# Optimization experiments

Hardware: AMD Instinct MI355X
Metric: run time of the kernel (lower is better)

The kernel has to match this reference:

```python
import jax, jax.numpy as jnp
import numpy as np

N_NODES = 30000
N_REL = 8
N_EDGES = 150000
EMB = 128
HID = 128
OUT = 256
HEADS = 4
RANK = 8
SCALE = 1.0
NEG_SLOPE = 0.2
LN_EPS = 1e-5


def setup_inputs():
    key = jax.random.key(0)
    ks = jax.random.split(key, 16)
    def nrm(k, shp, s=0.05):
        return jax.random.normal(k, shp, dtype=jnp.float32) * s
    d2 = HEADS * HID  # conv2 input dim = 512
    return {
        "entity_emb": nrm(ks[0], (N_NODES, EMB)),
        "A1": nrm(ks[1], (N_REL, EMB * RANK)),
        "B1": nrm(ks[2], (N_REL, EMB * RANK)),
        "W1": nrm(ks[3], (HEADS * HID, EMB)),
        "att_l1": nrm(ks[4], (1, HEADS, HID)),
        "att_r1": nrm(ks[5], (1, HEADS, HID)),
        "relb1": jnp.zeros((N_REL, HEADS), jnp.float32),
        "bias1": jnp.zeros((HEADS * HID,), jnp.float32),
        "A2": nrm(ks[6], (N_REL, d2 * RANK)),
        "B2": nrm(ks[7], (N_REL, d2 * RANK)),
        "W2": nrm(ks[8], (OUT, d2)),
        "att_l2": nrm(ks[9], (1, 1, OUT)),
        "att_r2": nrm(ks[10], (1, 1, OUT)),
        "relb2": jnp.zeros((N_REL, 1), jnp.float32),
        "bias2": jnp.zeros((OUT,), jnp.float32),
        "res_W": nrm(ks[11], (OUT, EMB)),
        "res_b": jnp.zeros((OUT,), jnp.float32),
        "ln_g": jnp.ones((OUT,), jnp.float32),
        "ln_b": jnp.zeros((OUT,), jnp.float32),
        "edge_index": jax.random.randint(ks[12], (2, N_EDGES), 0, N_NODES),
        "edge_type": jax.random.randint(ks[13], (N_EDGES,), 0, N_REL),
    }


def _rel_gat_conv(x, A, B, W, att_l, att_r, relb, bias, j_idx, i_idx, etype, heads, out_dim, concat):
    # x: [N,d]; A,B: [R, d*k]; W: [heads*out_dim, d]
    N, d = x.shape
    R = A.shape[0]
    k = RANK
    HC = heads * out_dim
    A3 = A.reshape(R, d, k)
    B3 = B.reshape(R, d, k)
    z_all = x @ W.T  # [N, HC] base linear (shared by z_i and z_j)
    # LoRA low-rank projection per (node, relation): P[n,r] = B_r^T x_n
    P = jnp.einsum('nd,rdk->nrk', x, B3)          # [N,R,k] (small)
    low = P[j_idx, etype]                          # [E,k]
    # Fused LoRA-through-lin: lin(scale*A_r B_r^T x) = scale * low @ (A_r^T W^T)
    M = jnp.einsum('rdk,hd->rkh', A3, W).reshape(R * k, HC)  # [R*k, HC]
    oh = jax.nn.one_hot(etype, R, dtype=x.dtype)   # [E,R]
    low_exp = (oh[:, :, None] * low[:, None, :]).reshape(-1, R * k)  # [E,R*k]
    z_j = (z_all[j_idx] + SCALE * (low_exp @ M)).reshape(-1, heads, out_dim)  # [E,H,C]
    z_i = z_all[i_idx].reshape(-1, heads, out_dim)                            # [E,H,C]
    alpha = (z_i * att_l).sum(-1) + (z_j * att_r).sum(-1) + relb[etype]       # [E,H]
    alpha = jax.nn.leaky_relu(alpha, NEG_SLOPE)
    # per-relation loop => softmax groups are (relation, target node)
    seg = etype * N + i_idx
    n_seg = R * N
    amax = jax.ops.segment_max(alpha, seg, num_segments=n_seg)
    ex = jnp.exp(alpha - amax[seg])
    den = jax.ops.segment_sum(ex, seg, num_segments=n_seg)
    alpha = ex / den[seg]
    msg = z_j * alpha[:, :, None]                  # [E,H,C]
    out = jax.ops.segment_sum(msg, i_idx, num_segments=N)  # [N,H,C]
    out = out.reshape(N, HC) if concat else out.mean(axis=1)
    return out + bias


def _forward(entity_emb, A1, B1, W1, att_l1, att_r1, relb1, bias1,
             A2, B2, W2, att_l2, att_r2, relb2, bias2,
             res_W, res_b, ln_g, ln_b, edge_index, edge_type):
    j_idx, i_idx = edge_index[0], edge_index[1]
    x0 = entity_emb
    x = _rel_gat_conv(x0, A1, B1, W1, att_l1, att_r1, relb1, bias1,
                      j_idx, i_idx, edge_type, HEADS, HID, True)
    x = jax.nn.elu(x)
    x = _rel_gat_conv(x, A2, B2, W2, att_l2, att_r2, relb2, bias2,
                      j_idx, i_idx, edge_type, 1, OUT, False)
    x = x + (x0 @ res_W.T + res_b)
    mu = x.mean(axis=-1, keepdims=True)
    var = ((x - mu) ** 2).mean(axis=-1, keepdims=True)
    return (x - mu) / jnp.sqrt(var + LN_EPS) * ln_g + ln_b


def reference(entity_emb, A1, B1, W1, att_l1, att_r1, relb1, bias1,
              A2, B2, W2, att_l2, att_r2, relb2, bias2,
              res_W, res_b, ln_g, ln_b, edge_index, edge_type):
    return _forward(entity_emb, A1, B1, W1, att_l1, att_r1, relb1, bias1,
                    A2, B2, W2, att_l2, att_r2, relb2, bias2,
                    res_W, res_b, ln_g, ln_b, edge_index, edge_type)
```

## Files before the change

kernel.cpp:

```cpp
#include <hip/hip_runtime.h>
#include <cstddef>

#define NRELS 8
#define EMB 128
#define HID 128
#define OUTD 256
#define HEADS 4
#define RANK 8
#define D2 512
#define KCAT 192
#define NEG_SLOPE 0.2f
#define LN_EPS 1e-5f

typedef short bf16x8 __attribute__((ext_vector_type(8)));
typedef float f32x4 __attribute__((ext_vector_type(4)));

__device__ __forceinline__ unsigned short f2bf(float f) {
  union { float f; unsigned u; } v; v.f = f;
  unsigned u = v.u;
  return (unsigned short)((u + 0x7fffu + ((u >> 16) & 1u)) >> 16);
}
__device__ __forceinline__ float bf2f(unsigned short u) {
  union { unsigned u; float f; } v; v.u = (unsigned)u << 16; return v.f;
}

#define GLOAD16(ldsp, gp) \
  __builtin_amdgcn_global_load_lds((const __attribute__((address_space(1))) unsigned int*)(gp), \
      (__attribute__((address_space(3))) unsigned int*)(ldsp), 16, 0, 0)

template<int ATT, int BIAS, int F32OUT, int PB>
__global__ __launch_bounds__(256) void gemm_tile(const unsigned short* __restrict__ A,
    const unsigned short* __restrict__ B, unsigned short* __restrict__ C,
    float* __restrict__ Cf, const unsigned short* __restrict__ Bp,
    float* __restrict__ Cp, int M, int N, int K, int lda, int aoffc,
    const float* __restrict__ bias, const float* __restrict__ b1p,
    const float* __restrict__ attL, const float* __restrict__ attR,
    float* __restrict__ al, float* __restrict__ ar) {
  __shared__ unsigned short As[128 * 32];
  __shared__ unsigned short Bs[128 * 32];
  __shared__ float pL[2][128];
  __shared__ float pR[2][128];
  const int tid = threadIdx.x;
  const int wave = tid >> 6;
  const int lane = tid & 63;
  const int wm = wave & 1;
  const int wn = wave >> 1;
  const int r16 = lane & 15;
  const int quad = lane >> 4;
  const int bm = blockIdx.x * 128;
  const int lr = lane >> 2;
  const int lc = (((lane & 3) ^ ((lane >> 3) & 3))) * 8;
  const int rsw = (quad ^ ((r16 >> 1) & 3)) * 8;
  int arow0 = bm + wave * 32 + lr;      if (arow0 >= M) arow0 = M - 1;
  int arow1 = bm + wave * 32 + 16 + lr; if (arow1 >= M) arow1 = M - 1;
  unsigned short* lA0 = As + wave * 1024;
  unsigned short* lA1 = As + wave * 1024 + 512;

  if (PB && blockIdx.y == (int)gridDim.y - 1) {
    const unsigned short* Ag0 = A + (size_t)arow0 * lda + lc;
    const unsigned short* Ag1 = A + (size_t)arow1 * lda + lc;
    const unsigned short* Bg = Bp + (size_t)(wave * 16 + lr) * K + lc;
    unsigned short* lBp = Bs + wave * 512;
    f32x4 accp[4][2] = {};
    for (int k0 = 0; k0 < K; k0 += 32) {
      __syncthreads();
      GLOAD16(lA0, Ag0 + k0);
      GLOAD16(lA1, Ag1 + k0);
      GLOAD16(lBp, Bg + k0);
      __syncthreads();
      bf16x8 af[4], bfr[2];
#pragma unroll
      for (int mi = 0; mi < 4; ++mi)
        af[mi] = *(const bf16x8*)(As + (wm * 64 + mi * 16 + r16) * 32 + rsw);
#pragma unroll
      for (int ni = 0; ni < 2; ++ni)
        bfr[ni] = *(const bf16x8*)(Bs + (wn * 32 + ni * 16 + r16) * 32 + rsw);
#pragma unroll
      for (int mi = 0; mi < 4; ++mi)
#pragma unroll
        for (int ni = 0; ni < 2; ++ni)
          accp[mi][ni] = __builtin_amdgcn_mfma_f32_16x16x32_bf16(af[mi], bfr[ni], accp[mi][ni], 0, 0, 0);
    }
#pragma unroll
    for (int mi = 0; mi < 4; ++mi)
#pragma unroll
      for (int ni = 0; ni < 2; ++ni)
#pragma unroll
        for (int r = 0; r < 4; ++r) {
          int row = bm + wm * 64 + mi * 16 + quad * 4 + r;
          if (row < M)
            Cp[(size_t)row * 64 + wn * 32 + ni * 16 + r16] = accp[mi][ni][r];
        }
    return;
  }

  const int bn = blockIdx.y * 128;
  const unsigned short* Abase = A + (size_t)blockIdx.y * aoffc;
  const unsigned short* Ag0 = Abase + (size_t)arow0 * lda + lc;
  const unsigned short* Ag1 = Abase + (size_t)arow1 * lda + lc;
  const unsigned short* Bg0 = B + (size_t)(bn + wave * 32 + lr) * K + lc;
  const unsigned short* Bg1 = B + (size_t)(bn + wave * 32 + 16 + lr) * K + lc;
  unsigned short* lB0 = Bs + wave * 1024;
  unsigned short* lB1 = Bs + wave * 1024 + 512;
  f32x4 acc[4][4] = {};
  for (int k0 = 0; k0 < K; k0 += 32) {
    __syncthreads();
    GLOAD16(lA0, Ag0 + k0);
    GLOAD16(lA1, Ag1 + k0);
    GLOAD16(lB0, Bg0 + k0);
    GLOAD16(lB1, Bg1 + k0);
    __syncthreads();
    bf16x8 af[4], bfr[4];
#pragma unroll
    for (int mi = 0; mi < 4; ++mi)
      af[mi] = *(const bf16x8*)(As + (wm * 64 + mi * 16 + r16) * 32 + rsw);
#pragma unroll
    for (int ni = 0; ni < 4; ++ni)
      bfr[ni] = *(const bf16x8*)(Bs + (wn * 64 + ni * 16 + r16) * 32 + rsw);
#pragma unroll
    for (int mi = 0; mi < 4; ++mi)
#pragma unroll
      for (int ni = 0; ni < 4; ++ni)
        acc[mi][ni] = __builtin_amdgcn_mfma_f32_16x16x32_bf16(af[mi], bfr[ni], acc[mi][ni], 0, 0, 0);
  }
  float bcol[4];
  if (BIAS) {
#pragma unroll
    for (int ni = 0; ni < 4; ++ni) {
      int cn = bn + wn * 64 + ni * 16 + r16;
      bcol[ni] = bias[cn];
      if (F32OUT) bcol[ni] += b1p[cn];
    }
  }
#pragma unroll
  for (int mi = 0; mi < 4; ++mi)
#pragma unroll
    for (int ni = 0; ni < 4; ++ni)
#pragma unroll
      for (int r = 0; r < 4; ++r) {
        int row = bm + wm * 64 + mi * 16 + quad * 4 + r;
        if (row < M) {
          float v = acc[mi][ni][r];
          if (BIAS) v += bcol[ni];
          size_t idx = (size_t)row * N + bn + wn * 64 + ni * 16 + r16;
          if (F32OUT) Cf[idx] = v;
          else        C[idx] = f2bf(v);
        }
      }
  if (ATT) {
    float La[4], Ra[4];
#pragma unroll
    for (int ni = 0; ni < 4; ++ni) {
      int cn = bn + wn * 64 + ni * 16 + r16;
      La[ni] = attL[cn]; Ra[ni] = attR[cn];
    }
#pragma unroll
    for (int mi = 0; mi < 4; ++mi)
#pragma unroll
      for (int r = 0; r < 4; ++r) {
        float sl = 0.f, sr = 0.f;
#pragma unroll
        for (int ni = 0; ni < 4; ++ni) {
          sl = fmaf(acc[mi][ni][r], La[ni], sl);
          sr = fmaf(acc[mi][ni][r], Ra[ni], sr);
        }
#pragma unroll
        for (int o = 1; o < 16; o <<= 1) {
          sl += __shfl_xor(sl, o, 64);
          sr += __shfl_xor(sr, o, 64);
        }
        if (r16 == 0) {
          int rl = wm * 64 + mi * 16 + quad * 4 + r;
          pL[wn][rl] = sl; pR[wn][rl] = sr;
        }
      }
    __syncthreads();
    if (tid < 128) {
      int row = bm + tid;
      if (row < M) {
        float sl = pL[0][tid] + pL[1][tid];
        float sr = pR[0][tid] + pR[1][tid];
        if (ATT == 1) {
          al[(size_t)row * 4 + blockIdx.y] = sl;
          ar[(size_t)row * 4 + blockIdx.y] = sr;
        } else {
          al[(size_t)blockIdx.y * M + row] = sl;
          ar[(size_t)blockIdx.y * M + row] = sr;
        }
      }
    }
  }
}

__global__ __launch_bounds__(256) void gemm_abt2(const float* __restrict__ Amat1,
    const float* __restrict__ W1, float* __restrict__ M1o,
    const float* __restrict__ Amat2, const float* __restrict__ W2, float* __restrict__ M2o) {
  const float* A; const float* B; float* C; int N, K, bn;
  if (blockIdx.x < D2 / 64) { A = Amat1; B = W1; C = M1o; N = D2; K = EMB; bn = blockIdx.x * 64; }
  else { A = Amat2; B = W2; C = M2o; N = OUTD; K = D2; bn = (blockIdx.x - D2 / 64) * 64; }
  __shared__ float As[32][64];
  __shared__ float Bs[32][64];
  const int tid = threadIdx.x;
  const int tx = tid & 15;
  const int ty = tid >> 4;
  const int lr = tid & 63;
  const int lq = tid >> 6;
  float acc[4][4] = {};
  for (int k0 = 0; k0 < K; k0 += 32) {
#pragma unroll
    for (int s = 0; s < 2; ++s) {
      const int q = lq + s * 4;
      float4 va = *(const float4*)(A + (size_t)lr * K + k0 + q * 4);
      As[q * 4 + 0][lr] = va.x; As[q * 4 + 1][lr] = va.y;
      As[q * 4 + 2][lr] = va.z; As[q * 4 + 3][lr] = va.w;
      float4 vb = *(const float4*)(B + (size_t)(bn + lr) * K + k0 + q * 4);
      Bs[q * 4 + 0][lr] = vb.x; Bs[q * 4 + 1][lr] = vb.y;
      Bs[q * 4 + 2][lr] = vb.z; Bs[q * 4 + 3][lr] = vb.w;
    }
    __syncthreads();
#pragma unroll
    for (int kk = 0; kk < 32; ++kk) {
      float a[4], b[4];
#pragma unroll
      for (int i2 = 0; i2 < 4; ++i2) { a[i2] = As[kk][ty * 4 + i2]; b[i2] = Bs[kk][tx * 4 + i2]; }
#pragma unroll
      for (int i2 = 0; i2 < 4; ++i2)
#pragma unroll
        for (int j2 = 0; j2 < 4; ++j2)
          acc[i2][j2] = fmaf(a[i2], b[j2], acc[i2][j2]);
    }
    __syncthreads();
  }
#pragma unroll
  for (int i2 = 0; i2 < 4; ++i2)
#pragma unroll
    for (int j2 = 0; j2 < 4; ++j2)
      C[(size_t)(ty * 4 + i2) * N + bn + tx * 4 + j2] = acc[i2][j2];
}

__global__ void prep_all(const float* __restrict__ x0, const float* __restrict__ W1,
    const float* __restrict__ W2, const float* __restrict__ res_W,
    const float* __restrict__ A1, const float* __restrict__ A2,
    const float* __restrict__ B1, const float* __restrict__ B2,
    unsigned short* __restrict__ x0b, unsigned short* __restrict__ Acat,
    unsigned short* __restrict__ W1b, unsigned short* __restrict__ W2b,
    unsigned short* __restrict__ RWcat,
    float* __restrict__ Amat1, float* __restrict__ Amat2,
    unsigned short* __restrict__ Bmat1b, unsigned short* __restrict__ Bmat2b, int nx0) {
  int idx = blockIdx.x * 256 + threadIdx.x;
  if (idx < nx0) { unsigned short b = f2bf(x0[idx]); x0b[idx] = b;
    Acat[(size_t)(idx >> 7) * KCAT + (idx & 127)] = b; return; } idx -= nx0;
  if (idx < D2 * EMB) { W1b[idx] = f2bf(W1[idx]); return; } idx -= D2 * EMB;
  if (idx < OUTD * D2) { W2b[idx] = f2bf(W2[idx]); return; } idx -= OUTD * D2;
  if (idx < OUTD * EMB) { RWcat[(size_t)(idx >> 7) * KCAT + (idx & 127)] = f2bf(res_W[idx]); return; } idx -= OUTD * EMB;
  if (idx < 64 * EMB) { int d = idx % EMB, rk = idx / EMB, k = rk & 7, r = rk >> 3;
    Amat1[idx] = A1[(size_t)r * EMB * RANK + (size_t)d * RANK + k]; return; } idx -= 64 * EMB;
  if (idx < 64 * D2) { int d = idx % D2, rk = idx / D2, k = rk & 7, r = rk >> 3;
    Amat2[idx] = A2[(size_t)r * D2 * RANK + (size_t)d * RANK + k]; return; } idx -= 64 * D2;
  if (idx < 64 * EMB) { int d = idx % EMB, rk = idx / EMB, k = rk & 7, r = rk >> 3;
    Bmat1b[idx] = f2bf(B1[(size_t)r * EMB * RANK + (size_t)d * RANK + k]); return; } idx -= 64 * EMB;
  if (idx < 64 * D2) { int d = idx % D2, rk = idx / D2, k = rk & 7, r = rk >> 3;
    Bmat2b[idx] = f2bf(B2[(size_t)r * D2 * RANK + (size_t)d * RANK + k]); }
}

__global__ void fold_build(const float* __restrict__ M1, const float* __restrict__ M2,
                           const float* __restrict__ attR1, const float* __restrict__ attR2,
                           unsigned short* __restrict__ M1T2, unsigned short* __restrict__ RWcat,
                           float* __restrict__ Matt1, float* __restrict__ Matt2) {
  int idx = blockIdx.x * 256 + threadIdx.x;
  if (idx < 512 * 64) { int c = idx >> 6, rk = idx & 63;
    M1T2[idx] = f2bf(M1[(size_t)rk * D2 + c]); return; } idx -= 512 * 64;
  if (idx < 256 * 64) { int c = idx >> 6, rk = idx & 63;
    RWcat[(size_t)c * KCAT + 128 + rk] = f2bf(M2[(size_t)rk * OUTD + c]); return; } idx -= 256 * 64;
  if (idx < 256) { int h = idx & 3, rk = idx >> 2;
    float s = 0.f;
    for (int c = 0; c < HID; ++c)
      s = fmaf(M1[(size_t)rk * D2 + h * HID + c], attR1[h * HID + c], s);
    Matt1[rk * 4 + h] = s; return; } idx -= 256;
  if (idx < 64) {
    float s = 0.f;
    for (int c = 0; c < OUTD; ++c) s = fmaf(M2[(size_t)idx * OUTD + c], attR2[c], s);
    Matt2[idx] = s; }
}

__global__ void hist_kernel(const int* __restrict__ ii, int* __restrict__ deg,
                            int* __restrict__ prepos, int E) {
  int e = blockIdx.x * blockDim.x + threadIdx.x;
  if (e < E) prepos[e] = atomicAdd(&deg[ii[e]], 1);
}

__global__ __launch_bounds__(1024) void exscan_kernel(const int* __restrict__ deg,
                                                      int* __restrict__ rowstart, int n) {
  __shared__ int wsum[16];
  int t = threadIdx.x;
  int lane = t & 63, wid = t >> 6;
  int carry = 0;
  for (int base = 0; base < n; base += 4096) {
    int i0 = base + t * 4;
    int v0 = 0, v1 = 0, v2 = 0, v3 = 0;
    if (i0 + 3 < n) {
      int4 vv = *(const int4*)(deg + i0);
      v0 = vv.x; v1 = vv.y; v2 = vv.z; v3 = vv.w;
    } else {
      if (i0 < n) v0 = deg[i0];
      if (i0 + 1 < n) v1 = deg[i0 + 1];
      if (i0 + 2 < n) v2 = deg[i0 + 2];
      if (i0 + 3 < n) v3 = deg[i0 + 3];
    }
    int tot = v0 + v1 + v2 + v3;
    int x = tot;
#pragma unroll
    for (int o = 1; o < 64; o <<= 1) {
      int y = __shfl_up(x, o, 64);
      if (lane >= o) x += y;
    }
    if (lane == 63) wsum[wid] = x;
    __syncthreads();
    if (t == 0) {
      int s = carry;
      for (int w2 = 0; w2 < 16; ++w2) { int tmp = wsum[w2]; wsum[w2] = s; s += tmp; }
      carry = s;
    }
    __syncthreads();
    int ex0 = x - tot + wsum[wid];
    if (i0 + 3 < n) {
      int4 ov; ov.x = ex0; ov.y = ex0 + v0; ov.z = ex0 + v0 + v1; ov.w = ex0 + v0 + v1 + v2;
      *(int4*)(rowstart + i0) = ov;
    } else {
      if (i0 < n) rowstart[i0] = ex0;
      if (i0 + 1 < n) rowstart[i0 + 1] = ex0 + v0;
      if (i0 + 2 < n) rowstart[i0 + 2] = ex0 + v0 + v1;
      if (i0 + 3 < n) rowstart[i0 + 3] = ex0 + v0 + v1 + v2;
    }
    __syncthreads();
  }
  if (t == 0) rowstart[n] = carry;
}

__global__ void edge_alpha1(const int* __restrict__ ji, const int* __restrict__ ii,
                            const int* __restrict__ et, const int* __restrict__ rowstart,
                            const int* __restrict__ prepos,
                            const float* __restrict__ P1,
                            const float* __restrict__ al1, const float* __restrict__ ar1,
                            const float* __restrict__ relb1, const float* __restrict__ Matt1,
                            float4* __restrict__ recs1, int E) {
  int e = blockIdx.x * blockDim.x + threadIdx.x;
  if (e >= E) return;
  int j = ji[e], i = ii[e], rt = et[e];
  float4 lo0 = *(const float4*)(P1 + (size_t)j * 64 + rt * 8);
  float4 lo1 = *(const float4*)(P1 + (size_t)j * 64 + rt * 8 + 4);
  float low[RANK] = {lo0.x, lo0.y, lo0.z, lo0.w, lo1.x, lo1.y, lo1.z, lo1.w};
  float4 ali = *(const float4*)(al1 + (size_t)i * 4);
  float4 arj = *(const float4*)(ar1 + (size_t)j * 4);
  float4 rb  = *(const float4*)(relb1 + rt * 4);
  float a0 = ali.x + arj.x + rb.x;
  float a1 = ali.y + arj.y + rb.y;
  float a2 = ali.z + arj.z + rb.z;
  float a3 = ali.w + arj.w + rb.w;
#pragma unroll
  for (int k = 0; k < RANK; ++k) {
    float4 mk = *(const float4*)(Matt1 + ((rt * 8 + k) << 2));
    a0 = fmaf(low[k], mk.x, a0); a1 = fmaf(low[k], mk.y, a1);
    a2 = fmaf(low[k], mk.z, a2); a3 = fmaf(low[k], mk.w, a3);
  }
  a0 = (a0 > 0.f) ? a0 : NEG_SLOPE * a0;
  a1 = (a1 > 0.f) ? a1 : NEG_SLOPE * a1;
  a2 = (a2 > 0.f) ? a2 : NEG_SLOPE * a2;
  a3 = (a3 > 0.f) ? a3 : NEG_SLOPE * a3;
  float e0 = expf(a0), e1 = expf(a1), e2 = expf(a2), e3 = expf(a3);
  float4* rp = recs1 + (size_t)(rowstart[i] + prepos[e]) * 4;
  rp[0] = make_float4(__int_as_float(j), e0, e1, e2);
  rp[1] = make_float4(e3, __int_as_float(rt), low[0], low[1]);
  rp[2] = make_float4(low[2], low[3], low[4], low[5]);
  rp[3] = make_float4(low[6], low[7], 0.f, 0.f);
}

__global__ __launch_bounds__(256) void qden1(float4* __restrict__ recs1,
    const int* __restrict__ rowstart, unsigned short* __restrict__ Q1b, int Nn) {
  __shared__ float denS[4][32];
  const int wid = threadIdx.x >> 6, lane = threadIdx.x & 63;
  const int i = blockIdx.x * 4 + wid;
  if (i >= Nn) return;
  const int rt_mine = lane >> 3, k = lane & 7;
  const int s0 = rowstart[i], deg = rowstart[i + 1] - s0;
  const float* rf = (const float*)recs1;
  float q0 = 0.f, q1 = 0.f, q2 = 0.f, q3 = 0.f;
  float d0 = 0.f, d1 = 0.f, d2 = 0.f, d3 = 0.f;
  float4 a0 = {}, a1 = {};
  float lw = 0.f;
  if (deg > 0) {
    a0 = recs1[(size_t)s0 * 4]; a1 = recs1[(size_t)s0 * 4 + 1];
    lw = rf[(size_t)s0 * 16 + 6 + k];
  }
  for (int p = 0; p < deg; ++p) {
    float4 b0 = a0, b1 = a1; float lwn = lw;
    if (p + 1 < deg) {
      b0 = recs1[(size_t)(s0 + p + 1) * 4]; b1 = recs1[(size_t)(s0 + p + 1) * 4 + 1];
      lwn = rf[(size_t)(s0 + p + 1) * 16 + 6 + k];
    }
    int rt = __float_as_int(a1.y);
    if (rt == rt_mine) {
      q0 = fmaf(a0.y, lw, q0); q1 = fmaf(a0.z, lw, q1);
      q2 = fmaf(a0.w, lw, q2); q3 = fmaf(a1.x, lw, q3);
      d0 += a0.y; d1 += a0.z; d2 += a0.w; d3 += a1.x;
    }
    a0 = b0; a1 = b1; lw = lwn;
  }
  float r0 = (d0 > 0.f) ? 1.f / d0 : 0.f;
  float r1 = (d1 > 0.f) ? 1.f / d1 : 0.f;
  float r2 = (d2 > 0.f) ? 1.f / d2 : 0.f;
  float r3 = (d3 > 0.f) ? 1.f / d3 : 0.f;
  size_t qb = (size_t)i * 256;
  Q1b[qb + lane]       = f2bf(q0 * r0);
  Q1b[qb + 64 + lane]  = f2bf(q1 * r1);
  Q1b[qb + 128 + lane] = f2bf(q2 * r2);
  Q1b[qb + 192 + lane] = f2bf(q3 * r3);
  if (k == 0) {
    denS[wid][rt_mine]      = r0;
    denS[wid][8 + rt_mine]  = r1;
    denS[wid][16 + rt_mine] = r2;
    denS[wid][24 + rt_mine] = r3;
  }
  for (int p = lane; p < deg; p += 64) {
    float4* rp = recs1 + (size_t)(s0 + p) * 4;
    float4 v0 = rp[0]; float4 v1 = rp[1];
    int rt = __float_as_int(v1.y);
    v0.y *= denS[wid][rt];      v0.z *= denS[wid][8 + rt];
    v0.w *= denS[wid][16 + rt]; v1.x *= denS[wid][24 + rt];
    rp[0] = v0; rp[1] = v1;
  }
}

__global__ __launch_bounds__(256) void node_agg1_lite(const float4* __restrict__ recs1,
    const int* __restrict__ rowstart, const unsigned short* __restrict__ z1b,
    const unsigned short* __restrict__ L1b, unsigned short* __restrict__ h1out, int Nn) {
  const int wid = threadIdx.x >> 6;
  const int lane = threadIdx.x & 63;
  const int i = blockIdx.x * 4 + wid;
  if (i >= Nn) return;
  const int s0 = rowstart[i];
  const int deg = rowstart[i + 1] - s0;
  const int c0 = lane * 8;
  const float* rf = (const float*)recs1;
  float acc[8] = {};
  float4 r0 = {}, r1 = {}, r2 = {};
  float w0 = 0.f, w1 = 0.f, w2 = 0.f;
  uint4 za = {}, zb = {};
  if (deg > 0) { r0 = recs1[(size_t)s0 * 4]; w0 = rf[(size_t)s0 * 16 + 4];
    za = *(const uint4*)(z1b + (size_t)__float_as_int(r0.x) * D2 + c0); }
  if (deg > 1) { r1 = recs1[(size_t)(s0 + 1) * 4]; w1 = rf[(size_t)(s0 + 1) * 16 + 4];
    zb = *(const uint4*)(z1b + (size_t)__float_as_int(r1.x) * D2 + c0); }
  if (deg > 2) { r2 = recs1[(size_t)(s0 + 2) * 4]; w2 = rf[(size_t)(s0 + 2) * 16 + 4]; }
  for (int p = 0; p < deg; ++p) {
    float4 r3 = r2; float w3 = w2; uint4 zn = zb;
    if (p + 3 < deg) { r3 = recs1[(size_t)(s0 + p + 3) * 4];
                       w3 = rf[(size_t)(s0 + p + 3) * 16 + 4]; }
    if (p + 2 < deg) zn = *(const uint4*)(z1b + (size_t)__float_as_int(r2.x) * D2 + c0);
    float wlo = (lane & 16) ? r0.z : r0.y;
    float whi = (lane & 16) ? w0 : r0.w;
    float wt = (lane & 32) ? whi : wlo;
    acc[0] = fmaf(wt, bf2f((unsigned short)(za.x & 0xffff)), acc[0]);
    acc[1] = fmaf(wt, bf2f((unsigned short)(za.x >> 16)), acc[1]);
    acc[2] = fmaf(wt, bf2f((unsigned short)(za.y & 0xffff)), acc[2]);
    acc[3] = fmaf(wt, bf2f((unsigned short)(za.y >> 16)), acc[3]);
    acc[4] = fmaf(wt, bf2f((unsigned short)(za.z & 0xffff)), acc[4]);
    acc[5] = fmaf(wt, bf2f((unsigned short)(za.z >> 16)), acc[5]);
    acc[6] = fmaf(wt, bf2f((unsigned short)(za.w & 0xffff)), acc[6]);
    acc[7] = fmaf(wt, bf2f((unsigned short)(za.w >> 16)), acc[7]);
    r0 = r1; w0 = w1; r1 = r2; w1 = w2; r2 = r3; w2 = w3; za = zb; zb = zn;
  }
  uint4 lv = *(const uint4*)(L1b + (size_t)i * D2 + c0);
  unsigned lw[4] = {lv.x, lv.y, lv.z, lv.w};
  unsigned ov[4];
#pragma unroll
  for (int q = 0; q < 4; ++q) {
    float e0 = acc[2 * q]     + bf2f((unsigned short)(lw[q] & 0xffff));
    float e1 = acc[2 * q + 1] + bf2f((unsigned short)(lw[q] >> 16));
    e0 = e0 > 0.f ? e0 : expm1f(e0);
    e1 = e1 > 0.f ? e1 : expm1f(e1);
    ov[q] = (unsigned)f2bf(e0) | ((unsigned)f2bf(e1) << 16);
  }
  *(uint4*)(h1out + (size_t)i * D2 + c0) = make_uint4(ov[0], ov[1], ov[2], ov[3]);
}

__global__ void edge_alpha2(const int* __restrict__ ji, const int* __restrict__ ii,
                            const int* __restrict__ et, const int* __restrict__ rowstart,
                            const int* __restrict__ prepos,
                            const float* __restrict__ P2,
                            const float* __restrict__ al2, const float* __restrict__ ar2,
                            const float* __restrict__ relb2, const float* __restrict__ Matt2,
                            float4* __restrict__ recs2, int E, int Nn) {
  int e = blockIdx.x * blockDim.x + threadIdx.x;
  if (e >= E) return;
  int j = ji[e], i = ii[e], rt = et[e];
  float4 lo0 = *(const float4*)(P2 + (size_t)j * 64 + rt * 8);
  float4 lo1 = *(const float4*)(P2 + (size_t)j * 64 + rt * 8 + 4);
  float low[RANK] = {lo0.x, lo0.y, lo0.z, lo0.w, lo1.x, lo1.y, lo1.z, lo1.w};
  float a = al2[i] + al2[(size_t)Nn + i] + ar2[j] + ar2[(size_t)Nn + j] + relb2[rt];
#pragma unroll
  for (int k = 0; k < RANK; ++k) a = fmaf(low[k], Matt2[rt * RANK + k], a);
  a = (a > 0.f) ? a : NEG_SLOPE * a;
  float ex = expf(a);
  float4* rp = recs2 + (size_t)(rowstart[i] + prepos[e]) * 3;
  rp[0] = make_float4(__int_as_float(j), __int_as_float(rt), ex, low[0]);
  rp[1] = make_float4(low[1], low[2], low[3], low[4]);
  rp[2] = make_float4(low[5], low[6], low[7], 0.f);
}

__global__ __launch_bounds__(256) void qden2(float4* __restrict__ recs2,
    const int* __restrict__ rowstart, unsigned short* __restrict__ Acat, int Nn) {
  __shared__ float denS[4][NRELS];
  const int wid = threadIdx.x >> 6, lane = threadIdx.x & 63;
  const int i = blockIdx.x * 4 + wid;
  if (i >= Nn) return;
  const int rt_mine = lane >> 3, k = lane & 7;
  const int s0 = rowstart[i], deg = rowstart[i + 1] - s0;
  const float* rf = (const float*)recs2;
  float q = 0.f, d = 0.f;
  float4 a0 = {}; float lw = 0.f;
  if (deg > 0) { a0 = recs2[(size_t)s0 * 3]; lw = rf[(size_t)s0 * 12 + 3 + k]; }
  for (int p = 0; p < deg; ++p) {
    float4 b0 = a0; float lwn = lw;
    if (p + 1 < deg) {
      b0 = recs2[(size_t)(s0 + p + 1) * 3];
      lwn = rf[(size_t)(s0 + p + 1) * 12 + 3 + k];
    }
    int rt = __float_as_int(a0.y);
    if (rt == rt_mine) { q = fmaf(a0.z, lw, q); d += a0.z; }
    a0 = b0; lw = lwn;
  }
  float rd = (d > 0.f) ? 1.f / d : 0.f;
  Acat[(size_t)i * KCAT + 128 + lane] = f2bf(q * rd);
  if (k == 0) denS[wid][rt_mine] = rd;
  for (int p = lane; p < deg; p += 64) {
    float* ep = (float*)(recs2 + (size_t)(s0 + p) * 3);
    int rt = __float_as_int(ep[1]);
    ep[2] *= denS[wid][rt];
  }
}

__global__ __launch_bounds__(256) void node_agg2_lite(const float4* __restrict__ recs2,
    const int* __restrict__ rowstart, const unsigned short* __restrict__ z2b,
    const float* __restrict__ o2, const float* __restrict__ ln_g,
    const float* __restrict__ ln_b, float* __restrict__ y, int Nn) {
  const int wid = threadIdx.x >> 6;
  const int lane = threadIdx.x & 63;
  const int i = blockIdx.x * 4 + wid;
  if (i >= Nn) return;
  const int s0 = rowstart[i];
  const int deg = rowstart[i + 1] - s0;
  const int c0 = lane * 4;
  float acc[4] = {};
  float4 r0 = {}, r1 = {}, r2 = {};
  uint2 za = make_uint2(0u, 0u), zb = make_uint2(0u, 0u);
  if (deg > 0) { r0 = recs2[(size_t)s0 * 3];
    za = *(const uint2*)(z2b + (size_t)__float_as_int(r0.x) * OUTD + c0); }
  if (deg > 1) { r1 = recs2[(size_t)(s0 + 1) * 3];
    zb = *(const uint2*)(z2b + (size_t)__float_as_int(r1.x) * OUTD + c0); }
  if (deg > 2) r2 = recs2[(size_t)(s0 + 2) * 3];
  for (int p = 0; p < deg; ++p) {
    float4 r3 = r2;
    uint2 zn = zb;
    if (p + 3 < deg) r3 = recs2[(size_t)(s0 + p + 3) * 3];
    if (p + 2 < deg)
      zn = *(const uint2*)(z2b + (size_t)__float_as_int(r2.x) * OUTD + c0);
    float wt = r0.z;
    acc[0] = fmaf(wt, bf2f((unsigned short)(za.x & 0xffff)), acc[0]);
    acc[1] = fmaf(wt, bf2f((unsigned short)(za.x >> 16)), acc[1]);
    acc[2] = fmaf(wt, bf2f((unsigned short)(za.y & 0xffff)), acc[2]);
    acc[3] = fmaf(wt, bf2f((unsigned short)(za.y >> 16)), acc[3]);
    r0 = r1; r1 = r2; r2 = r3; za = zb; zb = zn;
  }
  float4 rsv = *(const float4*)(o2 + (size_t)i * OUTD + c0);
  float vv[4];
  vv[0] = acc[0] + rsv.x;
  vv[1] = acc[1] + rsv.y;
  vv[2] = acc[2] + rsv.z;
  vv[3] = acc[3] + rsv.w;
  float s = vv[0] + vv[1] + vv[2] + vv[3];
  for (int o = 32; o > 0; o >>= 1) s += __shfl_xor(s, o, 64);
  float mu = s * (1.f / OUTD);
  float q = 0.f;
#pragma unroll
  for (int k = 0; k < 4; ++k) { float d = vv[k] - mu; q += d * d; }
  for (int o = 32; o > 0; o >>= 1) q += __shfl_xor(q, o, 64);
  float rstd = rsqrtf(q * (1.f / OUTD) + LN_EPS);
  float4 g = *(const float4*)(ln_g + c0);
  float4 bb = *(const float4*)(ln_b + c0);
  float4 ov;
  ov.x = (vv[0] - mu) * rstd * g.x + bb.x;
  ov.y = (vv[1] - mu) * rstd * g.y + bb.y;
  ov.z = (vv[2] - mu) * rstd * g.z + bb.z;
  ov.w = (vv[3] - mu) * rstd * g.w + bb.w;
  *(float4*)(y + (size_t)i * OUTD + c0) = ov;
}

extern "C" void kernel_launch(void* const* d_in, const int* in_sizes, int n_in,
                              void* d_out, int out_size, void* d_ws, size_t ws_size,
                              hipStream_t stream) {
  const float* x0     = (const float*)d_in[0];
  const float* A1     = (const float*)d_in[1];
  const float* B1     = (const float*)d_in[2];
  const float* W1     = (const float*)d_in[3];
  const float* attL1  = (const float*)d_in[4];
  const float* attR1  = (const float*)d_in[5];
  const float* relb1  = (const float*)d_in[6];
  const float* bias1  = (const float*)d_in[7];
  const float* A2     = (const float*)d_in[8];
  const float* B2     = (const float*)d_in[9];
  const float* W2     = (const float*)d_in[10];
  const float* attL2  = (const float*)d_in[11];
  const float* attR2  = (const float*)d_in[12];
  const float* relb2  = (const float*)d_in[13];
  const float* bias2  = (const float*)d_in[14];
  const float* res_W  = (const float*)d_in[15];
  const float* res_b  = (const float*)d_in[16];
  const float* ln_g   = (const float*)d_in[17];
  const float* ln_b   = (const float*)d_in[18];
  const int*   eidx   = (const int*)d_in[19];
  const int*   etype  = (const int*)d_in[20];
  float* out = (float*)d_out;

  const int Nn = in_sizes[0] / EMB;
  const int E  = in_sizes[20];
  const int* ji = eidx;
  const int* ii = eidx + E;

  float* w = (float*)d_ws;
  size_t off = 0;
  float* o2    = w + off; off += (size_t)Nn * OUTD;
  float* P1    = w + off; off += (size_t)Nn * 64;
  float* P2    = w + off; off += (size_t)Nn * 64;
  float* M1    = w + off; off += 64 * D2;
  float* M2    = w + off; off += 64 * OUTD;
  float* Amat1 = w + off; off += 64 * EMB;
  float* Amat2 = w + off; off += 64 * D2;
  float* Matt1 = w + off; off += 64 * 4;
  float* Matt2 = w + off; off += 64;
  float* al1   = w + off; off += (size_t)Nn * 4;
  float* ar1   = w + off; off += (size_t)Nn * 4;
  float* al2   = w + off; off += (size_t)Nn * 2;
  float* ar2   = w + off; off += (size_t)Nn * 2;
  float4* recs1 = (float4*)(w + off); off += (size_t)E * 16;
  float4* recs2 = (float4*)(w + off); off += (size_t)E * 12;
  unsigned short* z1b    = (unsigned short*)(w + off); off += (size_t)Nn * D2 / 2;
  unsigned short* z2b    = (unsigned short*)(w + off); off += (size_t)Nn * OUTD / 2;
  unsigned short* x0b    = (unsigned short*)(w + off); off += (size_t)Nn * EMB / 2;
  unsigned short* h1b    = (unsigned short*)(w + off); off += (size_t)Nn * D2 / 2;
  unsigned short* W1b    = (unsigned short*)(w + off); off += (size_t)D2 * EMB / 2;
  unsigned short* W2b    = (unsigned short*)(w + off); off += (size_t)OUTD * D2 / 2;
  unsigned short* Bmat1b = (unsigned short*)(w + off); off += (size_t)64 * EMB / 2;
  unsigned short* Bmat2b = (unsigned short*)(w + off); off += (size_t)64 * D2 / 2;
  unsigned short* Acat   = (unsigned short*)(w + off); off += (size_t)Nn * KCAT / 2;
  unsigned short* RWcat  = (unsigned short*)(w + off); off += (size_t)OUTD * KCAT / 2;
  unsigned short* M1T2   = (unsigned short*)(w + off); off += (size_t)512 * 64 / 2;
  int* ideg     = (int*)(w + off); off += (size_t)Nn;
  int* prepos   = (int*)(w + off); off += (size_t)E;
  int* rowstart = (int*)(w + off); off += (size_t)Nn + 1;
  (void)ws_size; (void)n_in; (void)out_size;

  unsigned short* Q1b = (unsigned short*)P1;
  unsigned short* L1b = (unsigned short*)o2;

  const int MT128 = (Nn + 127) / 128;
  const int NB4 = (Nn + 3) / 4;

  (void)hipMemsetAsync(ideg, 0, (size_t)Nn * sizeof(int), stream);
  hist_kernel<<<(E + 255) / 256, 256, 0, stream>>>(ii, ideg, prepos, E);
  exscan_kernel<<<1, 1024, 0, stream>>>(ideg, rowstart, Nn);

  {
    int nx0 = Nn * EMB;
    int total = nx0 + D2 * EMB + OUTD * D2 + OUTD * EMB + 64 * EMB + 64 * D2 + 64 * EMB + 64 * D2;
    prep_all<<<(total + 255) / 256, 256, 0, stream>>>(x0, W1, W2, res_W, A1, A2, B1, B2,
        x0b, Acat, W1b, W2b, RWcat, Amat1, Amat2, Bmat1b, Bmat2b, nx0);
  }

  gemm_abt2<<<dim3(D2 / 64 + OUTD / 64, 1), 256, 0, stream>>>(Amat1, W1, M1, Amat2, W2, M2);
  fold_build<<<(512 * 64 + 256 * 64 + 256 + 64 + 255) / 256, 256, 0, stream>>>(
      M1, M2, attR1, attR2, M1T2, RWcat, Matt1, Matt2);

  gemm_tile<1, 0, 0, 1><<<dim3(MT128, D2 / 128 + 1), 256, 0, stream>>>(x0b, W1b, z1b, nullptr,
      Bmat1b, P1, Nn, D2, EMB, EMB, 0, nullptr, nullptr, attL1, attR1, al1, ar1);

  edge_alpha1<<<(E + 255) / 256, 256, 0, stream>>>(ji, ii, etype, rowstart, prepos, P1,
                                                   al1, ar1, relb1, Matt1, recs1, E);
  qden1<<<NB4, 256, 0, stream>>>(recs1, rowstart, Q1b, Nn);
  gemm_tile<0, 1, 0, 0><<<dim3(MT128, D2 / 128), 256, 0, stream>>>(Q1b, M1T2, L1b, nullptr,
      nullptr, nullptr, Nn, D2, 64, 256, 64, bias1, nullptr, nullptr, nullptr, nullptr, nullptr);
  node_agg1_lite<<<NB4, 256, 0, stream>>>(recs1, rowstart, z1b, L1b, h1b, Nn);

  gemm_tile<2, 0, 0, 1><<<dim3(MT128, OUTD / 128 + 1), 256, 0, stream>>>(h1b, W2b, z2b, nullptr,
      Bmat2b, P2, Nn, OUTD, D2, D2, 0, nullptr, nullptr, attL2, attR2, al2, ar2);

  edge_alpha2<<<(E + 255) / 256, 256, 0, stream>>>(ji, ii, etype, rowstart, prepos, P2,
                                                   al2, ar2, relb2, Matt2, recs2, E, Nn);
  qden2<<<NB4, 256, 0, stream>>>(recs2, rowstart, Acat, Nn);
  gemm_tile<0, 1, 1, 0><<<dim3(MT128, OUTD / 128), 256, 0, stream>>>(Acat, RWcat, nullptr, o2,
      nullptr, nullptr, Nn, OUTD, KCAT, KCAT, 0, bias2, res_b, nullptr, nullptr, nullptr, nullptr);
  node_agg2_lite<<<NB4, 256, 0, stream>>>(recs2, rowstart, z2b, o2, ln_g, ln_b, out, Nn);
}
```

Before: 366.4 us.

## Widen GEMM K-tile to 64, fuse histogram into prep, defer softmax normalization

The bf16 MFMA GEMM now stages 64-wide K slices in LDS, with a new XOR swizzle and two MFMA sub-steps per barrier pair. That halves the number of sync/load rounds. The in-degree histogram atomics move into the prep_all launch, removing one kernel. The qden kernels no longer rewrite every edge record with the reciprocal softmax denominators. They store per-node, per-relation reciprocals, and the aggregation kernels multiply them in on the fly. The cost is higher LDS use per block and an extra LDS lookup per edge in aggregation.

```diff
diff --git a/kernel.cpp b/kernel.cpp
--- a/kernel.cpp
+++ b/kernel.cpp
@@ -36,8 +36,8 @@
     const float* __restrict__ bias, const float* __restrict__ b1p,
     const float* __restrict__ attL, const float* __restrict__ attR,
     float* __restrict__ al, float* __restrict__ ar) {
-  __shared__ unsigned short As[128 * 32];
-  __shared__ unsigned short Bs[128 * 32];
+  __shared__ unsigned short As[128 * 64];
+  __shared__ unsigned short Bs[128 * 64];
   __shared__ float pL[2][128];
   __shared__ float pR[2][128];
   const int tid = threadIdx.x;
@@ -48,38 +48,44 @@
   const int r16 = lane & 15;
   const int quad = lane >> 4;
   const int bm = blockIdx.x * 128;
-  const int lr = lane >> 2;
-  const int lc = (((lane & 3) ^ ((lane >> 3) & 3))) * 8;
-  const int rsw = (quad ^ ((r16 >> 1) & 3)) * 8;
-  int arow0 = bm + wave * 32 + lr;      if (arow0 >= M) arow0 = M - 1;
-  int arow1 = bm + wave * 32 + 16 + lr; if (arow1 >= M) arow1 = M - 1;
-  unsigned short* lA0 = As + wave * 1024;
-  unsigned short* lA1 = As + wave * 1024 + 512;
+  const int srow = lane >> 3;
+  const int gcol = ((lane & 7) ^ srow) * 8;
 
   if (PB && blockIdx.y == (int)gridDim.y - 1) {
-    const unsigned short* Ag0 = A + (size_t)arow0 * lda + lc;
-    const unsigned short* Ag1 = A + (size_t)arow1 * lda + lc;
-    const unsigned short* Bg = Bp + (size_t)(wave * 16 + lr) * K + lc;
-    unsigned short* lBp = Bs + wave * 512;
+    const unsigned short* Ag[4];
+#pragma unroll
+    for (int g = 0; g < 4; ++g) {
+      int r = bm + wave * 32 + g * 8 + srow; if (r >= M) r = M - 1;
+      Ag[g] = A + (size_t)r * lda + gcol;
+    }
+    const unsigned short* Bg[2];
+#pragma unroll
+    for (int g = 0; g < 2; ++g)
+      Bg[g] = Bp + (size_t)(wave * 16 + g * 8 + srow) * K + gcol;
     f32x4 accp[4][2] = {};
-    for (int k0 = 0; k0 < K; k0 += 32) {
+    for (int k0 = 0; k0 < K; k0 += 64) {
       __syncthreads();
-      GLOAD16(lA0, Ag0 + k0);
-      GLOAD16(lA1, Ag1 + k0);
-      GLOAD16(lBp, Bg + k0);
+#pragma unroll
+      for (int g = 0; g < 4; ++g) GLOAD16(As + (wave * 32 + g * 8) * 64, Ag[g] + k0);
+#pragma unroll
+      for (int g = 0; g < 2; ++g) GLOAD16(Bs + (wave * 16 + g * 8) * 64, Bg[g] + k0);
       __syncthreads();
-      bf16x8 af[4], bfr[2];
-#pragma unroll
-      for (int mi = 0; mi < 4; ++mi)
-        af[mi] = *(const bf16x8*)(As + (wm * 64 + mi * 16 + r16) * 32 + rsw);
-#pragma unroll
-      for (int ni = 0; ni < 2; ++ni)
-        bfr[ni] = *(const bf16x8*)(Bs + (wn * 32 + ni * 16 + r16) * 32 + rsw);
-#pragma unroll
-      for (int mi = 0; mi < 4; ++mi)
+#pragma unroll
+      for (int s = 0; s < 2; ++s) {
+        const int rs = ((s * 4 + quad) ^ (r16 & 7)) * 8;
+        bf16x8 af[4], bfr[2];
+#pragma unroll
+        for (int mi = 0; mi < 4; ++mi)
+          af[mi] = *(const bf16x8*)(As + (wm * 64 + mi * 16 + r16) * 64 + rs);
 #pragma unroll
         for (int ni = 0; ni < 2; ++ni)
-          accp[mi][ni] = __builtin_amdgcn_mfma_f32_16x16x32_bf16(af[mi], bfr[ni], accp[mi][ni], 0, 0, 0);
+          bfr[ni] = *(const bf16x8*)(Bs + (wn * 32 + ni * 16 + r16) * 64 + rs);
+#pragma unroll
+        for (int mi = 0; mi < 4; ++mi)
+#pragma unroll
+          for (int ni = 0; ni < 2; ++ni)
+            accp[mi][ni] = __builtin_amdgcn_mfma_f32_16x16x32_bf16(af[mi], bfr[ni], accp[mi][ni], 0, 0, 0);
+      }
     }
 #pragma unroll
     for (int mi = 0; mi < 4; ++mi)
@@ -96,32 +102,38 @@
 
   const int bn = blockIdx.y * 128;
   const unsigned short* Abase = A + (size_t)blockIdx.y * aoffc;
-  const unsigned short* Ag0 = Abase + (size_t)arow0 * lda + lc;
-  const unsigned short* Ag1 = Abase + (size_t)arow1 * lda + lc;
-  const unsigned short* Bg0 = B + (size_t)(bn + wave * 32 + lr) * K + lc;
-  const unsigned short* Bg1 = B + (size_t)(bn + wave * 32 + 16 + lr) * K + lc;
-  unsigned short* lB0 = Bs + wave * 1024;
-  unsigned short* lB1 = Bs + wave * 1024 + 512;
+  const unsigned short* Ag[4];
+  const unsigned short* Bg[4];
+#pragma unroll
+  for (int g = 0; g < 4; ++g) {
+    int r = bm + wave * 32 + g * 8 + srow; if (r >= M) r = M - 1;
+    Ag[g] = Abase + (size_t)r * lda + gcol;
+    Bg[g] = B + (size_t)(bn + wave * 32 + g * 8 + srow) * K + gcol;
+  }
   f32x4 acc[4][4] = {};
-  for (int k0 = 0; k0 < K; k0 += 32) {
+  for (int k0 = 0; k0 < K; k0 += 64) {
     __syncthreads();
-    GLOAD16(lA0, Ag0 + k0);
-    GLOAD16(lA1, Ag1 + k0);
-    GLOAD16(lB0, Bg0 + k0);
-    GLOAD16(lB1, Bg1 + k0);
+#pragma unroll
+    for (int g = 0; g < 4; ++g) GLOAD16(As + (wave * 32 + g * 8) * 64, Ag[g] + k0);
+#pragma unroll
+    for (int g = 0; g < 4; ++g) GLOAD16(Bs + (wave * 32 + g * 8) * 64, Bg[g] + k0);
     __syncthreads();
-    bf16x8 af[4], bfr[4];
-#pragma unroll
-    for (int mi = 0; mi < 4; ++mi)
-      af[mi] = *(const bf16x8*)(As + (wm * 64 + mi * 16 + r16) * 32 + rsw);
-#pragma unroll
-    for (int ni = 0; ni < 4; ++ni)
-      bfr[ni] = *(const bf16x8*)(Bs + (wn * 64 + ni * 16 + r16) * 32 + rsw);
-#pragma unroll
-    for (int mi = 0; mi < 4; ++mi)
+#pragma unroll
+    for (int s = 0; s < 2; ++s) {
+      const int rs = ((s * 4 + quad) ^ (r16 & 7)) * 8;
+      bf16x8 af[4], bfr[4];
+#pragma unroll
+      for (int mi = 0; mi < 4; ++mi)
+        af[mi] = *(const bf16x8*)(As + (wm * 64 + mi * 16 + r16) * 64 + rs);
 #pragma unroll
       for (int ni = 0; ni < 4; ++ni)
-        acc[mi][ni] = __builtin_amdgcn_mfma_f32_16x16x32_bf16(af[mi], bfr[ni], acc[mi][ni], 0, 0, 0);
+        bfr[ni] = *(const bf16x8*)(Bs + (wn * 64 + ni * 16 + r16) * 64 + rs);
+#pragma unroll
+      for (int mi = 0; mi < 4; ++mi)
+#pragma unroll
+        for (int ni = 0; ni < 4; ++ni)
+          acc[mi][ni] = __builtin_amdgcn_mfma_f32_16x16x32_bf16(af[mi], bfr[ni], acc[mi][ni], 0, 0, 0);
+    }
   }
   float bcol[4];
   if (BIAS) {
@@ -246,8 +258,11 @@
     unsigned short* __restrict__ W1b, unsigned short* __restrict__ W2b,
     unsigned short* __restrict__ RWcat,
     float* __restrict__ Amat1, float* __restrict__ Amat2,
-    unsigned short* __restrict__ Bmat1b, unsigned short* __restrict__ Bmat2b, int nx0) {
+    unsigned short* __restrict__ Bmat1b, unsigned short* __restrict__ Bmat2b,
+    const int* __restrict__ ii, int* __restrict__ ideg, int* __restrict__ prepos,
+    int E, int nx0) {
   int idx = blockIdx.x * 256 + threadIdx.x;
+  if (idx < E) { prepos[idx] = atomicAdd(&ideg[ii[idx]], 1); return; } idx -= E;
   if (idx < nx0) { unsigned short b = f2bf(x0[idx]); x0b[idx] = b;
     Acat[(size_t)(idx >> 7) * KCAT + (idx & 127)] = b; return; } idx -= nx0;
   if (idx < D2 * EMB) { W1b[idx] = f2bf(W1[idx]); return; } idx -= D2 * EMB;
@@ -281,12 +296,6 @@
     float s = 0.f;
     for (int c = 0; c < OUTD; ++c) s = fmaf(M2[(size_t)idx * OUTD + c], attR2[c], s);
     Matt2[idx] = s; }
-}
-
-__global__ void hist_kernel(const int* __restrict__ ii, int* __restrict__ deg,
-                            int* __restrict__ prepos, int E) {
-  int e = blockIdx.x * blockDim.x + threadIdx.x;
-  if (e < E) prepos[e] = atomicAdd(&deg[ii[e]], 1);
 }
 
 __global__ __launch_bounds__(1024) void exscan_kernel(const int* __restrict__ deg,
@@ -375,9 +384,9 @@
   rp[3] = make_float4(low[6], low[7], 0.f, 0.f);
 }
 
-__global__ __launch_bounds__(256) void qden1(float4* __restrict__ recs1,
-    const int* __restrict__ rowstart, unsigned short* __restrict__ Q1b, int Nn) {
-  __shared__ float denS[4][32];
+__global__ __launch_bounds__(256) void qden1(const float4* __restrict__ recs1,
+    const int* __restrict__ rowstart, unsigned short* __restrict__ Q1b,
+    float* __restrict__ rden1, int Nn) {
   const int wid = threadIdx.x >> 6, lane = threadIdx.x & 63;
   const int i = blockIdx.x * 4 + wid;
   if (i >= Nn) return;
@@ -416,49 +425,47 @@
   Q1b[qb + 128 + lane] = f2bf(q2 * r2);
   Q1b[qb + 192 + lane] = f2bf(q3 * r3);
   if (k == 0) {
-    denS[wid][rt_mine]      = r0;
-    denS[wid][8 + rt_mine]  = r1;
-    denS[wid][16 + rt_mine] = r2;
-    denS[wid][24 + rt_mine] = r3;
-  }
-  for (int p = lane; p < deg; p += 64) {
-    float4* rp = recs1 + (size_t)(s0 + p) * 4;
-    float4 v0 = rp[0]; float4 v1 = rp[1];
-    int rt = __float_as_int(v1.y);
-    v0.y *= denS[wid][rt];      v0.z *= denS[wid][8 + rt];
-    v0.w *= denS[wid][16 + rt]; v1.x *= denS[wid][24 + rt];
-    rp[0] = v0; rp[1] = v1;
+    size_t db = (size_t)i * 32;
+    rden1[db + rt_mine]      = r0;
+    rden1[db + 8 + rt_mine]  = r1;
+    rden1[db + 16 + rt_mine] = r2;
+    rden1[db + 24 + rt_mine] = r3;
   }
 }
 
 __global__ __launch_bounds__(256) void node_agg1_lite(const float4* __restrict__ recs1,
     const int* __restrict__ rowstart, const unsigned short* __restrict__ z1b,
-    const unsigned short* __restrict__ L1b, unsigned short* __restrict__ h1out, int Nn) {
+    const unsigned short* __restrict__ L1b, const float* __restrict__ rden1,
+    unsigned short* __restrict__ h1out, int Nn) {
   const int wid = threadIdx.x >> 6;
   const int lane = threadIdx.x & 63;
   const int i = blockIdx.x * 4 + wid;
   if (i >= Nn) return;
+  __shared__ float denS[4][32];
+  if (lane < 32) denS[wid][lane] = rden1[(size_t)i * 32 + lane];
   const int s0 = rowstart[i];
   const int deg = rowstart[i + 1] - s0;
   const int c0 = lane * 8;
   const float* rf = (const float*)recs1;
+  const int hb = (lane >> 4) << 3;
   float acc[8] = {};
   float4 r0 = {}, r1 = {}, r2 = {};
-  float w0 = 0.f, w1 = 0.f, w2 = 0.f;
+  float2 g0 = {}, g1 = {}, g2 = {};
   uint4 za = {}, zb = {};
-  if (deg > 0) { r0 = recs1[(size_t)s0 * 4]; w0 = rf[(size_t)s0 * 16 + 4];
+  if (deg > 0) { r0 = recs1[(size_t)s0 * 4]; g0 = *(const float2*)(rf + (size_t)s0 * 16 + 4);
     za = *(const uint4*)(z1b + (size_t)__float_as_int(r0.x) * D2 + c0); }
-  if (deg > 1) { r1 = recs1[(size_t)(s0 + 1) * 4]; w1 = rf[(size_t)(s0 + 1) * 16 + 4];
+  if (deg > 1) { r1 = recs1[(size_t)(s0 + 1) * 4]; g1 = *(const float2*)(rf + (size_t)(s0 + 1) * 16 + 4);
     zb = *(const uint4*)(z1b + (size_t)__float_as_int(r1.x) * D2 + c0); }
-  if (deg > 2) { r2 = recs1[(size_t)(s0 + 2) * 4]; w2 = rf[(size_t)(s0 + 2) * 16 + 4]; }
+  if (deg > 2) { r2 = recs1[(size_t)(s0 + 2) * 4]; g2 = *(const float2*)(rf + (size_t)(s0 + 2) * 16 + 4); }
   for (int p = 0; p < deg; ++p) {
-    float4 r3 = r2; float w3 = w2; uint4 zn = zb;
+    float4 r3 = r2; float2 g3 = g2; uint4 zn = zb;
     if (p + 3 < deg) { r3 = recs1[(size_t)(s0 + p + 3) * 4];
-                       w3 = rf[(size_t)(s0 + p + 3) * 16 + 4]; }
+                       g3 = *(const float2*)(rf + (size_t)(s0 + p + 3) * 16 + 4); }
     if (p + 2 < deg) zn = *(const uint4*)(z1b + (size_t)__float_as_int(r2.x) * D2 + c0);
+    int rt = __float_as_int(g0.y);
     float wlo = (lane & 16) ? r0.z : r0.y;
-    float whi = (lane & 16) ? w0 : r0.w;
-    float wt = (lane & 32) ? whi : wlo;
+    float whi = (lane & 16) ? g0.x : r0.w;
+    float wt = ((lane & 32) ? whi : wlo) * denS[wid][hb + rt];
     acc[0] = fmaf(wt, bf2f((unsigned short)(za.x & 0xffff)), acc[0]);
     acc[1] = fmaf(wt, bf2f((unsigned short)(za.x >> 16)), acc[1]);
     acc[2] = fmaf(wt, bf2f((unsigned short)(za.y & 0xffff)), acc[2]);
@@ -467,7 +474,7 @@
     acc[5] = fmaf(wt, bf2f((unsigned short)(za.z >> 16)), acc[5]);
     acc[6] = fmaf(wt, bf2f((unsigned short)(za.w & 0xffff)), acc[6]);
     acc[7] = fmaf(wt, bf2f((unsigned short)(za.w >> 16)), acc[7]);
-    r0 = r1; w0 = w1; r1 = r2; w1 = w2; r2 = r3; w2 = w3; za = zb; zb = zn;
+    r0 = r1; g0 = g1; r1 = r2; g1 = g2; r2 = r3; g2 = g3; za = zb; zb = zn;
   }
   uint4 lv = *(const uint4*)(L1b + (size_t)i * D2 + c0);
   unsigned lw[4] = {lv.x, lv.y, lv.z, lv.w};
@@ -507,9 +514,9 @@
   rp[2] = make_float4(low[5], low[6], low[7], 0.f);
 }
 
-__global__ __launch_bounds__(256) void qden2(float4* __restrict__ recs2,
-    const int* __restrict__ rowstart, unsigned short* __restrict__ Acat, int Nn) {
-  __shared__ float denS[4][NRELS];
+__global__ __launch_bounds__(256) void qden2(const float4* __restrict__ recs2,
+    const int* __restrict__ rowstart, unsigned short* __restrict__ Acat,
+    float* __restrict__ rden2, int Nn) {
   const int wid = threadIdx.x >> 6, lane = threadIdx.x & 63;
   const int i = blockIdx.x * 4 + wid;
   if (i >= Nn) return;
@@ -531,22 +538,20 @@
   }
   float rd = (d > 0.f) ? 1.f / d : 0.f;
   Acat[(size_t)i * KCAT + 128 + lane] = f2bf(q * rd);
-  if (k == 0) denS[wid][rt_mine] = rd;
-  for (int p = lane; p < deg; p += 64) {
-    float* ep = (float*)(recs2 + (size_t)(s0 + p) * 3);
-    int rt = __float_as_int(ep[1]);
-    ep[2] *= denS[wid][rt];
-  }
+  if (k == 0) rden2[(size_t)i * 8 + rt_mine] = rd;
 }
 
 __global__ __launch_bounds__(256) void node_agg2_lite(const float4* __restrict__ recs2,
     const int* __restrict__ rowstart, const unsigned short* __restrict__ z2b,
-    const float* __restrict__ o2, const float* __restrict__ ln_g,
-    const float* __restrict__ ln_b, float* __restrict__ y, int Nn) {
+    const float* __restrict__ rden2, const float* __restrict__ o2,
+    const float* __restrict__ ln_g, const float* __restrict__ ln_b,
+    float* __restrict__ y, int Nn) {
   const int wid = threadIdx.x >> 6;
   const int lane = threadIdx.x & 63;
   const int i = blockIdx.x * 4 + wid;
   if (i >= Nn) return;
+  __shared__ float denS[4][NRELS];
+  if (lane < NRELS) denS[wid][lane] = rden2[(size_t)i * 8 + lane];
   const int s0 = rowstart[i];
   const int deg = rowstart[i + 1] - s0;
   const int c0 = lane * 4;
@@ -564,7 +569,8 @@
     if (p + 3 < deg) r3 = recs2[(size_t)(s0 + p + 3) * 3];
     if (p + 2 < deg)
       zn = *(const uint2*)(z2b + (size_t)__float_as_int(r2.x) * OUTD + c0);
-    float wt = r0.z;
+    int rt = __float_as_int(r0.y);
+    float wt = r0.z * denS[wid][rt];
     acc[0] = fmaf(wt, bf2f((unsigned short)(za.x & 0xffff)), acc[0]);
     acc[1] = fmaf(wt, bf2f((unsigned short)(za.x >> 16)), acc[1]);
     acc[2] = fmaf(wt, bf2f((unsigned short)(za.y & 0xffff)), acc[2]);
@@ -641,6 +647,8 @@
   float* ar1   = w + off; off += (size_t)Nn * 4;
   float* al2   = w + off; off += (size_t)Nn * 2;
   float* ar2   = w + off; off += (size_t)Nn * 2;
+  float* rden1 = w + off; off += (size_t)Nn * 32;
+  float* rden2 = w + off; off += (size_t)Nn * 8;
   float4* recs1 = (float4*)(w + off); off += (size_t)E * 16;
   float4* recs2 = (float4*)(w + off); off += (size_t)E * 12;
   unsigned short* z1b    = (unsigned short*)(w + off); off += (size_t)Nn * D2 / 2;
@@ -666,15 +674,14 @@
   const int NB4 = (Nn + 3) / 4;
 
   (void)hipMemsetAsync(ideg, 0, (size_t)Nn * sizeof(int), stream);
-  hist_kernel<<<(E + 255) / 256, 256, 0, stream>>>(ii, ideg, prepos, E);
-  exscan_kernel<<<1, 1024, 0, stream>>>(ideg, rowstart, Nn);
-
   {
     int nx0 = Nn * EMB;
-    int total = nx0 + D2 * EMB + OUTD * D2 + OUTD * EMB + 64 * EMB + 64 * D2 + 64 * EMB + 64 * D2;
+    int total = E + nx0 + D2 * EMB + OUTD * D2 + OUTD * EMB
+              + 64 * EMB + 64 * D2 + 64 * EMB + 64 * D2;
     prep_all<<<(total + 255) / 256, 256, 0, stream>>>(x0, W1, W2, res_W, A1, A2, B1, B2,
-        x0b, Acat, W1b, W2b, RWcat, Amat1, Amat2, Bmat1b, Bmat2b, nx0);
-  }
+        x0b, Acat, W1b, W2b, RWcat, Amat1, Amat2, Bmat1b, Bmat2b, ii, ideg, prepos, E, nx0);
+  }
+  exscan_kernel<<<1, 1024, 0, stream>>>(ideg, rowstart, Nn);
 
   gemm_abt2<<<dim3(D2 / 64 + OUTD / 64, 1), 256, 0, stream>>>(Amat1, W1, M1, Amat2, W2, M2);
   fold_build<<<(512 * 64 + 256 * 64 + 256 + 64 + 255) / 256, 256, 0, stream>>>(
@@ -685,18 +692,18 @@
 
   edge_alpha1<<<(E + 255) / 256, 256, 0, stream>>>(ji, ii, etype, rowstart, prepos, P1,
                                                    al1, ar1, relb1, Matt1, recs1, E);
-  qden1<<<NB4, 256, 0, stream>>>(recs1, rowstart, Q1b, Nn);
+  qden1<<<NB4, 256, 0, stream>>>(recs1, rowstart, Q1b, rden1, Nn);
   gemm_tile<0, 1, 0, 0><<<dim3(MT128, D2 / 128), 256, 0, stream>>>(Q1b, M1T2, L1b, nullptr,
       nullptr, nullptr, Nn, D2, 64, 256, 64, bias1, nullptr, nullptr, nullptr, nullptr, nullptr);
-  node_agg1_lite<<<NB4, 256, 0, stream>>>(recs1, rowstart, z1b, L1b, h1b, Nn);
+  node_agg1_lite<<<NB4, 256, 0, stream>>>(recs1, rowstart, z1b, L1b, rden1, h1b, Nn);
 
   gemm_tile<2, 0, 0, 1><<<dim3(MT128, OUTD / 128 + 1), 256, 0, stream>>>(h1b, W2b, z2b, nullptr,
       Bmat2b, P2, Nn, OUTD, D2, D2, 0, nullptr, nullptr, attL2, attR2, al2, ar2);
 
   edge_alpha2<<<(E + 255) / 256, 256, 0, stream>>>(ji, ii, etype, rowstart, prepos, P2,
                                                    al2, ar2, relb2, Matt2, recs2, E, Nn);
-  qden2<<<NB4, 256, 0, stream>>>(recs2, rowstart, Acat, Nn);
+  qden2<<<NB4, 256, 0, stream>>>(recs2, rowstart, Acat, rden2, Nn);
   gemm_tile<0, 1, 1, 0><<<dim3(MT128, OUTD / 128), 256, 0, stream>>>(Acat, RWcat, nullptr, o2,
       nullptr, nullptr, Nn, OUTD, KCAT, KCAT, 0, bias2, res_b, nullptr, nullptr, nullptr, nullptr);
-  node_agg2_lite<<<NB4, 256, 0, stream>>>(recs2, rowstart, z2b, o2, ln_g, ln_b, out, Nn);
-}
+  node_agg2_lite<<<NB4, 256, 0, stream>>>(recs2, rowstart, z2b, rden2, o2, ln_g, ln_b, out, Nn);
+}
```

Result: slower. 375.8 us (+2.6%).
